# Performance work log

Measured on AMD Instinct MI355X. Metric: run time of the kernel, lower is better.

## Reference

```python
import jax, jax.numpy as jnp
import numpy as np


def _graph_conv(src, dst, x, num_nodes, inv_sqrt_out, inv_sqrt_in):
    # DGL GraphConv, norm='both': h = D_in^{-1/2} A D_out^{-1/2} x
    msg = (x * inv_sqrt_out[:, None])[src]                      # [E, F] gather
    agg = jax.ops.segment_sum(msg, dst, num_segments=num_nodes)  # [N, F] scatter-add
    return agg * inv_sqrt_in[:, None]


def setup_inputs() -> dict:
    key = jax.random.key(0)
    ks = jax.random.split(key, 8)
    N, E, IN, H, C = 4096, 131072, 512, 8192, 16
    return {
        "features": jax.random.normal(ks[0], (N, IN), dtype=jnp.float32),
        "W1": jax.random.normal(ks[1], (IN, H), dtype=jnp.float32) * 0.02,
        "b1": jnp.zeros((H,), dtype=jnp.float32),
        "W2": jax.random.normal(ks[2], (H, N), dtype=jnp.float32) * 0.02,
        "Wl": jax.random.normal(ks[3], (N, C), dtype=jnp.float32) * 0.02,
        "bl": jnp.zeros((C,), dtype=jnp.float32),
        "src": jax.random.randint(ks[4], (E,), 0, N, dtype=jnp.int32),
        "dst": jax.random.randint(ks[5], (E,), 0, N, dtype=jnp.int32),
    }


def reference(features, W1, b1, W2, Wl, bl, src, dst):
    N = features.shape[0]
    ones = jnp.ones(src.shape, dtype=features.dtype)
    deg_out = jnp.clip(jax.ops.segment_sum(ones, src, num_segments=N), 1.0)
    deg_in = jnp.clip(jax.ops.segment_sum(ones, dst, num_segments=N), 1.0)
    inv_sqrt_out = jax.lax.rsqrt(deg_out)
    inv_sqrt_in = jax.lax.rsqrt(deg_in)

    # conv1: project then aggregate (math identical to DGL's ordering)
    x = features @ W1 + b1
    x = _graph_conv(src, dst, x, N, inv_sqrt_out, inv_sqrt_in)   # [N, 2N]
    # dropout: identity in inference mode
    # conv2 (weight passed externally, no bias)
    x = x @ W2
    x = _graph_conv(src, dst, x, N, inv_sqrt_out, inv_sqrt_in)   # [N, N]
    x = jax.nn.relu(x)
    x = x @ Wl + bl                                              # [N, C]
    return jax.nn.softmax(x, axis=1)
```

## Files before the change

### kernel.cpp

```cpp
#include <hip/hip_runtime.h>
#include <cstdint>
#include <cstddef>


using bf8   = __attribute__((ext_vector_type(8))) short;
using s4    = __attribute__((ext_vector_type(4))) short;
using f32x4 = __attribute__((ext_vector_type(4))) float;

static __device__ __forceinline__ unsigned short f2bf(float f) {
    union { float f; uint32_t u; } v; v.f = f;
    uint32_t r = (v.u + 0x7FFFu + ((v.u >> 16) & 1u)) >> 16;
    return (unsigned short)r;
}
static __device__ __forceinline__ float bf2f(unsigned short b) {
    union { uint32_t u; float f; } v; v.u = ((uint32_t)b) << 16;
    return v.f;
}

static __device__ __forceinline__ void gload16(const short* g, short* l) {
    __builtin_amdgcn_global_load_lds(
        (const __attribute__((address_space(1))) unsigned int*)g,
        (__attribute__((address_space(3))) unsigned int*)l,
        16, 0, 0);
}


__global__ void k_zero(float* a, float* b, int* c, int n) {
    int i = blockIdx.x * blockDim.x + threadIdx.x;
    if (i < n) { a[i] = 0.f; b[i] = 0.f; c[i] = 0; }
}

__global__ void k_count(const int* __restrict__ src, const int* __restrict__ dst,
                        float* deg_out, float* deg_in, int E) {
    int e = blockIdx.x * blockDim.x + threadIdx.x;
    if (e < E) {
        atomicAdd(&deg_out[src[e]], 1.f);
        atomicAdd(&deg_in[dst[e]], 1.f);
    }
}

__global__ void k_inv(const float* deg_out, const float* deg_in,
                      float* inv_out, float* inv_in, int n) {
    int i = blockIdx.x * blockDim.x + threadIdx.x;
    if (i < n) {
        inv_out[i] = rsqrtf(fmaxf(deg_out[i], 1.f));
        inv_in[i]  = rsqrtf(fmaxf(deg_in[i], 1.f));
    }
}

__global__ void k_scan(const float* __restrict__ deg_in, int* __restrict__ row_off) {
    __shared__ int part[1024];
    const int t = threadIdx.x;
    int v0 = (int)deg_in[t*4+0], v1 = (int)deg_in[t*4+1],
        v2 = (int)deg_in[t*4+2], v3 = (int)deg_in[t*4+3];
    part[t] = v0 + v1 + v2 + v3;
    __syncthreads();
    for (int off = 1; off < 1024; off <<= 1) {
        int x = (t >= off) ? part[t - off] : 0;
        __syncthreads();
        part[t] += x;
        __syncthreads();
    }
    int run = (t == 0) ? 0 : part[t-1];
    row_off[t*4+0] = run; run += v0;
    row_off[t*4+1] = run; run += v1;
    row_off[t*4+2] = run; run += v2;
    row_off[t*4+3] = run; run += v3;
    if (t == 1023) row_off[4096] = run;
}

__global__ void k_fill(const int* __restrict__ src, const int* __restrict__ dst,
                       const int* __restrict__ row_off, int* cursor,
                       int* __restrict__ esrc, int E) {
    int e = blockIdx.x * blockDim.x + threadIdx.x;
    if (e < E) {
        int d = dst[e];
        int p = atomicAdd(&cursor[d], 1);
        esrc[row_off[d] + p] = src[e];
    }
}

__global__ void k_rowsum(const int* __restrict__ row_off, const int* __restrict__ esrc,
                         const float* __restrict__ inv_out, const float* __restrict__ inv_in,
                         float* __restrict__ rowsum) {
    const int node = blockIdx.x, lane = threadIdx.x;
    const int beg = row_off[node], end = row_off[node + 1];
    float s = 0.f;
    for (int p = beg + lane; p < end; p += 64) s += inv_out[esrc[p]];
    #pragma unroll
    for (int off = 32; off; off >>= 1) s += __shfl_down(s, off, 64);
    if (lane == 0) rowsum[node] = s * inv_in[node];
}

__global__ void k_cvt_scale(const float* __restrict__ in, const float* __restrict__ sc,
                            short* __restrict__ out, int n4, int f4) {
    int i = blockIdx.x * blockDim.x + threadIdx.x;
    if (i < n4) {
        const float s = sc[i / f4];
        float4 v = reinterpret_cast<const float4*>(in)[i];
        s4 o;
        o[0] = (short)f2bf(v.x * s); o[1] = (short)f2bf(v.y * s);
        o[2] = (short)f2bf(v.z * s); o[3] = (short)f2bf(v.w * s);
        reinterpret_cast<s4*>(out)[i] = o;
    }
}

__global__ void k_tr2(const float* __restrict__ in, short* __restrict__ out, int R, int C) {
    __shared__ float tile[64][33];
    const int bc = blockIdx.x * 32, br = blockIdx.y * 64;
    const int tx = threadIdx.x, ty = threadIdx.y;
    #pragma unroll
    for (int dy = 0; dy < 64; dy += 8)
        tile[ty + dy][tx] = in[(size_t)(br + ty + dy) * C + bc + tx];
    __syncthreads();
    #pragma unroll
    for (int dy = 0; dy < 32; dy += 8) {
        const int oy = ty + dy;
        ushort2 o;
        o.x = f2bf(tile[tx * 2][oy]);
        o.y = f2bf(tile[tx * 2 + 1][oy]);
        *reinterpret_cast<ushort2*>(&out[(size_t)(bc + oy) * R + br + tx * 2]) = o;
    }
}

template<int EPI>
__global__ __launch_bounds__(512, 2)
void gemm8p(const short* __restrict__ A, const short* __restrict__ Bt,
            short* __restrict__ C,
            const float* __restrict__ bias, const float* __restrict__ rs,
            int M, int N, int K)
{
    constexpr int USZ  = 4096;
    constexpr int BOFF = 4 * USZ;
    constexpr int BUF  = 8 * USZ;
    __shared__ __align__(16) short lds[2 * BUF];
    const int tid  = threadIdx.x;
    const int wid  = tid >> 6, lane = tid & 63;
    const int wm   = wid >> 2;
    const int wn   = wid & 3;
    const int fr   = lane & 15;
    const int kq   = lane >> 4;
    const int nt   = K >> 6;

    const int gx  = gridDim.x;
    const int nwg = gx * gridDim.y;
    int bid = blockIdx.y * gx + blockIdx.x;
    bid = (bid & 7) * (nwg >> 3) + (bid >> 3);
    const int tm = (bid / gx) * 256;
    const int tn = (bid % gx) * 256;

    const int srow = tid >> 3;
    const int scq  = tid & 7;
    const int scs  = scq ^ (srow & 7);
    const short* gA = A  + (size_t)(tm + srow) * K + scs * 8;
    const short* gB = Bt + (size_t)(tn + srow) * K + scs * 8;
    short* const ldst = lds + tid * 8;

    const int cx0 = (0 * 4 + kq) ^ (fr & 7);
    const int cx1 = (1 * 4 + kq) ^ (fr & 7);
    int aoff[8][2], boff[4][2];
    #pragma unroll
    for (int mi = 0; mi < 8; ++mi) {
        const int r = wm * 128 + mi * 16 + fr;
        aoff[mi][0] = r * 64 + cx0 * 8;
        aoff[mi][1] = r * 64 + cx1 * 8;
    }
    #pragma unroll
    for (int n = 0; n < 4; ++n) {
        const int r = wn * 64 + n * 16 + fr;
        boff[n][0] = BOFF + r * 64 + cx0 * 8;
        boff[n][1] = BOFF + r * 64 + cx1 * 8;
    }

    f32x4 acc[8][4];
    #pragma unroll
    for (int mi = 0; mi < 8; ++mi)
        #pragma unroll
        for (int n = 0; n < 4; ++n)
            acc[mi][n] = (f32x4){0.f, 0.f, 0.f, 0.f};

    #pragma unroll
    for (int u = 0; u < 4; ++u) gload16(gA + (size_t)u * 64 * K, ldst + u * USZ);
    #pragma unroll
    for (int v = 0; v < 4; ++v) gload16(gB + (size_t)v * 64 * K, ldst + BOFF + v * USZ);
    #pragma unroll
    for (int u = 0; u < 4; ++u) gload16(gA + (size_t)u * 64 * K + 64, ldst + BUF + u * USZ);
    #pragma unroll
    for (int v = 0; v < 4; ++v) gload16(gB + (size_t)v * 64 * K + 64, ldst + BUF + BOFF + v * USZ);
    asm volatile("s_waitcnt vmcnt(8)" ::: "memory");
    __builtin_amdgcn_sched_barrier(0);
    __builtin_amdgcn_s_barrier();

    for (int t = 0; t < nt; ++t) {
        const int cc = (t & 1) * BUF;
        const bool pf = (t + 2 < nt);
        const size_t kf = (size_t)(t + 2) * 64;

        bf8 a03[4][2], a47[4][2], bg[4][2];

        #pragma unroll
        for (int mi = 0; mi < 4; ++mi)
            #pragma unroll
            for (int s = 0; s < 2; ++s)
                a03[mi][s] = *reinterpret_cast<const bf8*>(lds + cc + aoff[mi][s]);
        #pragma unroll
        for (int n = 0; n < 2; ++n)
            #pragma unroll
            for (int s = 0; s < 2; ++s)
                bg[n][s] = *reinterpret_cast<const bf8*>(lds + cc + boff[n][s]);
        __builtin_amdgcn_s_barrier();
        asm volatile("s_waitcnt lgkmcnt(0)" ::: "memory");
        __builtin_amdgcn_sched_barrier(0);
        __builtin_amdgcn_s_setprio(1);
        #pragma unroll
        for (int mi = 0; mi < 4; ++mi)
            #pragma unroll
            for (int n = 0; n < 2; ++n)
                #pragma unroll
                for (int s = 0; s < 2; ++s)
                    acc[mi][n] = __builtin_amdgcn_mfma_f32_16x16x32_bf16(a03[mi][s], bg[n][s], acc[mi][n], 0, 0, 0);
        __builtin_amdgcn_s_setprio(0);
        __builtin_amdgcn_s_barrier();

        #pragma unroll
        for (int n = 2; n < 4; ++n)
            #pragma unroll
            for (int s = 0; s < 2; ++s)
                bg[n][s] = *reinterpret_cast<const bf8*>(lds + cc + boff[n][s]);
        __builtin_amdgcn_s_barrier();
        asm volatile("s_waitcnt lgkmcnt(0)" ::: "memory");
        __builtin_amdgcn_sched_barrier(0);
        __builtin_amdgcn_s_setprio(1);
        #pragma unroll
        for (int mi = 0; mi < 4; ++mi)
            #pragma unroll
            for (int n = 2; n < 4; ++n)
                #pragma unroll
                for (int s = 0; s < 2; ++s)
                    acc[mi][n] = __builtin_amdgcn_mfma_f32_16x16x32_bf16(a03[mi][s], bg[n][s], acc[mi][n], 0, 0, 0);
        __builtin_amdgcn_s_setprio(0);
        __builtin_amdgcn_s_barrier();

        #pragma unroll
        for (int mi = 0; mi < 4; ++mi)
            #pragma unroll
            for (int s = 0; s < 2; ++s)
                a47[mi][s] = *reinterpret_cast<const bf8*>(lds + cc + aoff[4 + mi][s]);
        if (pf) {
            #pragma unroll
            for (int v = 0; v < 4; ++v)
                gload16(gB + (size_t)v * 64 * K + kf, ldst + cc + BOFF + v * USZ);
        }
        __builtin_amdgcn_s_barrier();
        asm volatile("s_waitcnt lgkmcnt(0)" ::: "memory");
        __builtin_amdgcn_sched_barrier(0);
        __builtin_amdgcn_s_setprio(1);
        #pragma unroll
        for (int mi = 0; mi < 4; ++mi)
            #pragma unroll
            for (int n = 0; n < 2; ++n)
                #pragma unroll
                for (int s = 0; s < 2; ++s)
                    acc[4 + mi][n] = __builtin_amdgcn_mfma_f32_16x16x32_bf16(a47[mi][s], bg[n][s], acc[4 + mi][n], 0, 0, 0);
        __builtin_amdgcn_s_setprio(0);
        __builtin_amdgcn_s_barrier();

        if (pf) {
            #pragma unroll
            for (int u = 0; u < 4; ++u)
                gload16(gA + (size_t)u * 64 * K + kf, ldst + cc + u * USZ);
        }
        __builtin_amdgcn_s_setprio(1);
        #pragma unroll
        for (int mi = 0; mi < 4; ++mi)
            #pragma unroll
            for (int n = 2; n < 4; ++n)
                #pragma unroll
                for (int s = 0; s < 2; ++s)
                    acc[4 + mi][2 + (n - 2)] = acc[4 + mi][n];
        #pragma unroll
        for (int mi = 0; mi < 4; ++mi)
            #pragma unroll
            for (int n = 2; n < 4; ++n)
                #pragma unroll
                for (int s = 0; s < 2; ++s)
                    acc[4 + mi][n] = __builtin_amdgcn_mfma_f32_16x16x32_bf16(a47[mi][s], bg[n][s], acc[4 + mi][n], 0, 0, 0);
        __builtin_amdgcn_s_setprio(0);
        if (pf) {
            asm volatile("s_waitcnt vmcnt(8)" ::: "memory");
        } else if (t + 2 == nt) {
            asm volatile("s_waitcnt vmcnt(0)" ::: "memory");
        }
        __builtin_amdgcn_sched_barrier(0);
        __builtin_amdgcn_s_barrier();
    }

    const int rb = kq * 4;
    #pragma unroll
    for (int mi = 0; mi < 8; ++mi) {
        #pragma unroll
        for (int n = 0; n < 4; ++n) {
            const int col = tn + wn * 64 + n * 16 + fr;
            const float bcol = (EPI == 1) ? bias[col] : 0.f;
            #pragma unroll
            for (int j = 0; j < 4; ++j) {
                const int row = tm + wm * 128 + mi * 16 + rb + j;
                float v = acc[mi][n][j];
                if (EPI == 1) v += rs[row] * bcol;
                else          v *= rs[row];
                C[(size_t)row * N + col] = (short)f2bf(v);
            }
        }
    }
}

template<int RELU>
__global__ __launch_bounds__(64)
void agg_strip(const short* __restrict__ X, short* __restrict__ Y,
               const int* __restrict__ row_off, const int* __restrict__ esrc,
               const float* __restrict__ inv_in, int F)
{
    const int node = blockIdx.y;
    const int c0 = blockIdx.x * 512 + threadIdx.x * 8;
    float acc[8];
    #pragma unroll
    for (int j = 0; j < 8; ++j) acc[j] = 0.f;

    const int beg = row_off[node], end = row_off[node + 1];
    int p = beg;
    for (; p + 3 < end; p += 4) {
        const int s0 = esrc[p], s1 = esrc[p + 1], s2 = esrc[p + 2], s3 = esrc[p + 3];
        bf8 x0 = *reinterpret_cast<const bf8*>(X + (size_t)s0 * F + c0);
        bf8 x1 = *reinterpret_cast<const bf8*>(X + (size_t)s1 * F + c0);
        bf8 x2 = *reinterpret_cast<const bf8*>(X + (size_t)s2 * F + c0);
        bf8 x3 = *reinterpret_cast<const bf8*>(X + (size_t)s3 * F + c0);
        #pragma unroll
        for (int j = 0; j < 8; ++j)
            acc[j] += (bf2f((unsigned short)x0[j]) + bf2f((unsigned short)x1[j]))
                    + (bf2f((unsigned short)x2[j]) + bf2f((unsigned short)x3[j]));
    }
    for (; p < end; ++p) {
        const int s0 = esrc[p];
        bf8 x0 = *reinterpret_cast<const bf8*>(X + (size_t)s0 * F + c0);
        #pragma unroll
        for (int j = 0; j < 8; ++j) acc[j] += bf2f((unsigned short)x0[j]);
    }
    const float sc = inv_in[node];
    bf8 o;
    #pragma unroll
    for (int j = 0; j < 8; ++j) {
        float v = acc[j] * sc;
        if (RELU) v = fmaxf(v, 0.f);
        o[j] = (short)f2bf(v);
    }
    *reinterpret_cast<bf8*>(Y + (size_t)node * F + c0) = o;
}

__global__ __launch_bounds__(256)
void k_headgemm(const short* __restrict__ H, const float* __restrict__ Wl,
                float* __restrict__ logitsP)
{
    constexpr int RS = 520;
    __shared__ __align__(16) short ldsB[16 * RS];
    const int tid = threadIdx.x;
    const int m0  = blockIdx.x * 256;
    const int k0  = blockIdx.y * 512;
    const int wid = tid >> 6, lane = tid & 63;
    const int fr  = lane & 15;
    const int kq  = lane >> 4;

    {
        const int c = tid & 15, kk = tid >> 4;
        #pragma unroll
        for (int j = 0; j < 32; ++j) {
            const int k = kk * 32 + j;
            ldsB[c * RS + k] = (short)f2bf(Wl[(size_t)(k0 + k) * 16 + c]);
        }
    }
    __syncthreads();

    const int rb0 = m0 + wid * 64;
    f32x4 acc[4];
    #pragma unroll
    for (int mi = 0; mi < 4; ++mi) acc[mi] = (f32x4){0.f, 0.f, 0.f, 0.f};

    #pragma unroll 4
    for (int s = 0; s < 16; ++s) {
        const bf8 b = *reinterpret_cast<const bf8*>(ldsB + fr * RS + s * 32 + kq * 8);
        #pragma unroll
        for (int mi = 0; mi < 4; ++mi) {
            const bf8 a = *reinterpret_cast<const bf8*>(
                H + (size_t)(rb0 + mi * 16 + fr) * 4096 + k0 + s * 32 + kq * 8);
            acc[mi] = __builtin_amdgcn_mfma_f32_16x16x32_bf16(a, b, acc[mi], 0, 0, 0);
        }
    }

    float* outP = logitsP + (size_t)blockIdx.y * 4096 * 16;
    #pragma unroll
    for (int mi = 0; mi < 4; ++mi)
        #pragma unroll
        for (int j = 0; j < 4; ++j)
            outP[(size_t)(rb0 + mi * 16 + kq * 4 + j) * 16 + fr] = acc[mi][j];
}

__global__ __launch_bounds__(64)
void k_soft(const float* __restrict__ logitsP, const float* __restrict__ bl,
            float* __restrict__ out)
{
    const int node = blockIdx.x * 64 + threadIdx.x;
    float l[16];
    #pragma unroll
    for (int c = 0; c < 16; ++c) l[c] = bl[c];
    for (int p = 0; p < 8; ++p) {
        const float4* lp = reinterpret_cast<const float4*>(
            logitsP + ((size_t)p * 4096 + node) * 16);
        #pragma unroll
        for (int q = 0; q < 4; ++q) {
            float4 v = lp[q];
            l[q*4+0] += v.x; l[q*4+1] += v.y; l[q*4+2] += v.z; l[q*4+3] += v.w;
        }
    }
    float mx = l[0];
    #pragma unroll
    for (int c = 1; c < 16; ++c) mx = fmaxf(mx, l[c]);
    float s = 0.f;
    #pragma unroll
    for (int c = 0; c < 16; ++c) { l[c] = expf(l[c] - mx); s += l[c]; }
    const float inv = 1.f / s;
    float4* o = reinterpret_cast<float4*>(out + (size_t)node * 16);
    #pragma unroll
    for (int q = 0; q < 4; ++q)
        o[q] = make_float4(l[q*4+0]*inv, l[q*4+1]*inv, l[q*4+2]*inv, l[q*4+3]*inv);
}


extern "C" void kernel_launch(void* const* d_in, const int* in_sizes, int n_in,
                              void* d_out, int out_size, void* d_ws, size_t ws_size,
                              hipStream_t stream)
{
    const float* features = (const float*)d_in[0];
    const float* W1       = (const float*)d_in[1];
    const float* b1       = (const float*)d_in[2];
    const float* W2       = (const float*)d_in[3];
    const float* Wl       = (const float*)d_in[4];
    const float* bl       = (const float*)d_in[5];
    const int*   src      = (const int*)d_in[6];
    const int*   dst      = (const int*)d_in[7];
    float* out = (float*)d_out;

    const int N = 4096, IN = 512, H = 8192;
    const int E = in_sizes[6];

    char* ws = (char*)d_ws;
    size_t o = 0;
    auto alloc = [&](size_t bytes) -> char* {
        char* p = ws + o;
        o = (o + bytes + 255) & ~(size_t)255;
        return p;
    };
    short* W2t   = (short*)alloc((size_t)N * H * 2);
    short* h1    = (short*)alloc((size_t)N * H * 2);
    short* x2s   = (short*)alloc((size_t)N * N * 2);
    short* featb = (short*)alloc((size_t)N * IN * 2);
    short* aggF  = (short*)alloc((size_t)N * IN * 2);
    short* W1t   = (short*)alloc((size_t)H * IN * 2);
    float* logitsP = (float*)alloc((size_t)8 * N * 16 * 4);
    float* deg_out = (float*)alloc(N * 4);
    float* deg_in  = (float*)alloc(N * 4);
    float* inv_out = (float*)alloc(N * 4);
    float* inv_in  = (float*)alloc(N * 4);
    float* rowsum  = (float*)alloc(N * 4);
    int*   cursor  = (int*)alloc(N * 4);
    int*   row_off = (int*)alloc((N + 1) * 4);
    int*   esrc    = (int*)alloc((size_t)E * 4);
    short* h2 = h1;

    k_zero <<<(N + 255) / 256, 256, 0, stream>>>(deg_out, deg_in, cursor, N);
    k_count<<<(E + 255) / 256, 256, 0, stream>>>(src, dst, deg_out, deg_in, E);
    k_inv  <<<(N + 255) / 256, 256, 0, stream>>>(deg_out, deg_in, inv_out, inv_in, N);
    k_scan <<<1, 1024, 0, stream>>>(deg_in, row_off);
    k_fill <<<(E + 255) / 256, 256, 0, stream>>>(src, dst, row_off, cursor, esrc, E);
    k_rowsum<<<N, 64, 0, stream>>>(row_off, esrc, inv_out, inv_in, rowsum);

    k_cvt_scale<<<(N * IN / 4 + 255) / 256, 256, 0, stream>>>(features, inv_out, featb,
                                                              N * IN / 4, IN / 4);
    k_tr2<<<dim3(H / 32, IN / 64), dim3(32, 8), 0, stream>>>(W1, W1t, IN, H);
    k_tr2<<<dim3(N / 32, H / 64), dim3(32, 8), 0, stream>>>(W2, W2t, H, N);

    agg_strip<0><<<dim3(1, N), 64, 0, stream>>>(featb, aggF, row_off, esrc, inv_in, IN);
    gemm8p<1><<<dim3(H / 256, N / 256), 512, 0, stream>>>(aggF, W1t, h1, b1, rowsum, N, H, IN);

    gemm8p<2><<<dim3(N / 256, N / 256), 512, 0, stream>>>(h1, W2t, x2s, nullptr, inv_out, N, N, H);
    agg_strip<1><<<dim3(N / 512, N), 64, 0, stream>>>(x2s, h2, row_off, esrc, inv_in, N);

    k_headgemm<<<dim3(N / 256, 8), 256, 0, stream>>>(h2, Wl, logitsP);
    k_soft<<<N / 64, 64, 0, stream>>>(logitsP, bl, out);
}
```

Baseline: 434.2 us.

## Widen weight transpose tiles, deepen gather unroll, drop redundant accumulator copies

Replaces the 32x64 transpose kernel with a 64x64 tile version that uses float4 global loads and 4-wide bf16 stores, cutting the instruction count of converting W1 and W2 (the W2 transpose moves a large fp32 matrix). Removes a leftover loop in the GEMM main loop that copied accumulator registers before the second MFMA group; those copies were redundant and could cost moves or register pressure. Raises the aggregation gather unroll from 4 to 8 edges so more independent loads are in flight, at the cost of more registers and a longer remainder loop. Summation order in the aggregation changes slightly.

New measurement: 433.1 us. About the same (-0.2%).

```diff
diff --git a/kernel.cpp b/kernel.cpp
--- a/kernel.cpp
+++ b/kernel.cpp
@@ -105,21 +105,30 @@
     }
 }
 
-__global__ void k_tr2(const float* __restrict__ in, short* __restrict__ out, int R, int C) {
-    __shared__ float tile[64][33];
-    const int bc = blockIdx.x * 32, br = blockIdx.y * 64;
-    const int tx = threadIdx.x, ty = threadIdx.y;
-    #pragma unroll
-    for (int dy = 0; dy < 64; dy += 8)
-        tile[ty + dy][tx] = in[(size_t)(br + ty + dy) * C + bc + tx];
+__global__ __launch_bounds__(256)
+void k_tr3(const float* __restrict__ in, short* __restrict__ out, int R, int C) {
+    __shared__ float tile[64][65];
+    const int bc = blockIdx.x * 64, br = blockIdx.y * 64;
+    const int t = threadIdx.x;
+    const int rr = t >> 4, cq = (t & 15) * 4;
+    #pragma unroll
+    for (int p = 0; p < 4; ++p) {
+        const int r = rr + p * 16;
+        float4 v = *reinterpret_cast<const float4*>(&in[(size_t)(br + r) * C + bc + cq]);
+        tile[r][cq + 0] = v.x; tile[r][cq + 1] = v.y;
+        tile[r][cq + 2] = v.z; tile[r][cq + 3] = v.w;
+    }
     __syncthreads();
-    #pragma unroll
-    for (int dy = 0; dy < 32; dy += 8) {
-        const int oy = ty + dy;
-        ushort2 o;
-        o.x = f2bf(tile[tx * 2][oy]);
-        o.y = f2bf(tile[tx * 2 + 1][oy]);
-        *reinterpret_cast<ushort2*>(&out[(size_t)(bc + oy) * R + br + tx * 2]) = o;
+    const int cc = t >> 4, rq = (t & 15) * 4;
+    #pragma unroll
+    for (int p = 0; p < 4; ++p) {
+        const int c = cc + p * 16;
+        s4 o;
+        o[0] = (short)f2bf(tile[rq + 0][c]);
+        o[1] = (short)f2bf(tile[rq + 1][c]);
+        o[2] = (short)f2bf(tile[rq + 2][c]);
+        o[3] = (short)f2bf(tile[rq + 3][c]);
+        *reinterpret_cast<s4*>(&out[(size_t)(bc + c) * R + br + rq]) = o;
     }
 }
 
@@ -277,13 +286,6 @@
             for (int n = 2; n < 4; ++n)
                 #pragma unroll
                 for (int s = 0; s < 2; ++s)
-                    acc[4 + mi][2 + (n - 2)] = acc[4 + mi][n];
-        #pragma unroll
-        for (int mi = 0; mi < 4; ++mi)
-            #pragma unroll
-            for (int n = 2; n < 4; ++n)
-                #pragma unroll
-                for (int s = 0; s < 2; ++s)
                     acc[4 + mi][n] = __builtin_amdgcn_mfma_f32_16x16x32_bf16(a47[mi][s], bg[n][s], acc[4 + mi][n], 0, 0, 0);
         __builtin_amdgcn_s_setprio(0);
         if (pf) {
@@ -328,20 +330,19 @@
 
     const int beg = row_off[node], end = row_off[node + 1];
     int p = beg;
-    for (; p + 3 < end; p += 4) {
-        const int s0 = esrc[p], s1 = esrc[p + 1], s2 = esrc[p + 2], s3 = esrc[p + 3];
-        bf8 x0 = *reinterpret_cast<const bf8*>(X + (size_t)s0 * F + c0);
-        bf8 x1 = *reinterpret_cast<const bf8*>(X + (size_t)s1 * F + c0);
-        bf8 x2 = *reinterpret_cast<const bf8*>(X + (size_t)s2 * F + c0);
-        bf8 x3 = *reinterpret_cast<const bf8*>(X + (size_t)s3 * F + c0);
-        #pragma unroll
-        for (int j = 0; j < 8; ++j)
-            acc[j] += (bf2f((unsigned short)x0[j]) + bf2f((unsigned short)x1[j]))
-                    + (bf2f((unsigned short)x2[j]) + bf2f((unsigned short)x3[j]));
+    for (; p + 7 < end; p += 8) {
+        bf8 x[8];
+        #pragma unroll
+        for (int u = 0; u < 8; ++u)
+            x[u] = *reinterpret_cast<const bf8*>(X + (size_t)esrc[p + u] * F + c0);
+        #pragma unroll
+        for (int u = 0; u < 8; ++u)
+            #pragma unroll
+            for (int j = 0; j < 8; ++j)
+                acc[j] += bf2f((unsigned short)x[u][j]);
     }
     for (; p < end; ++p) {
-        const int s0 = esrc[p];
-        bf8 x0 = *reinterpret_cast<const bf8*>(X + (size_t)s0 * F + c0);
+        bf8 x0 = *reinterpret_cast<const bf8*>(X + (size_t)esrc[p] * F + c0);
         #pragma unroll
         for (int j = 0; j < 8; ++j) acc[j] += bf2f((unsigned short)x0[j]);
     }
@@ -484,8 +485,8 @@
 
     k_cvt_scale<<<(N * IN / 4 + 255) / 256, 256, 0, stream>>>(features, inv_out, featb,
                                                               N * IN / 4, IN / 4);
-    k_tr2<<<dim3(H / 32, IN / 64), dim3(32, 8), 0, stream>>>(W1, W1t, IN, H);
-    k_tr2<<<dim3(N / 32, H / 64), dim3(32, 8), 0, stream>>>(W2, W2t, H, N);
+    k_tr3<<<dim3(H / 64, IN / 64), 256, 0, stream>>>(W1, W1t, IN, H);
+    k_tr3<<<dim3(N / 64, H / 64), 256, 0, stream>>>(W2, W2t, H, N);
 
     agg_strip<0><<<dim3(1, N), 64, 0, stream>>>(featb, aggF, row_off, esrc, inv_in, IN);
     gemm8p<1><<<dim3(H / 256, N / 256), 512, 0, stream>>>(aggF, W1t, h1, b1, rowsum, N, H, IN);
```
